# Performance work log

Hardware: AMD Instinct MI355X
Metric: run time of the kernel (lower is better)

The kernel has to match this reference:

```python
import jax, jax.numpy as jnp
import numpy as np

EPS = 1e-3
LOG2PI = float(np.log(2.0 * np.pi))

# dims
B, Z, Y, T, D = 32768, 256, 32, 64, 4  # batch, z_dim, y_dim, n_types, type_dim


def setup_inputs() -> dict:
    key = jax.random.key(0)
    ks = jax.random.split(key, 8)
    z = jax.random.normal(ks[0], (B, Z), dtype=jnp.float32)
    batch_x = jax.random.normal(ks[1], (B, T, D), dtype=jnp.float32)
    miss_list = jax.random.randint(ks[2], (B, T), 0, 2, dtype=jnp.int32)  # 1=observed, 0=missing
    data_mean = jax.random.normal(ks[3], (T, D), dtype=jnp.float32)
    data_var = jax.random.uniform(ks[4], (T, D), dtype=jnp.float32, minval=0.5, maxval=1.5)
    # weights init N(0, 0.005) as in the torch module; biases zero
    Wy = jax.random.normal(ks[5], (T * Y, Z), dtype=jnp.float32) * 0.005
    by = jnp.zeros((T * Y,), dtype=jnp.float32)
    Wm = jax.random.normal(ks[6], (T, D, Y), dtype=jnp.float32) * 0.005
    bm = jnp.zeros((T, D), dtype=jnp.float32)
    Wv = jax.random.normal(ks[7], (T, D, Y), dtype=jnp.float32) * 0.005
    bv = jnp.zeros((T, D), dtype=jnp.float32)
    return {"z": z, "batch_x": batch_x, "miss_list": miss_list,
            "data_mean": data_mean, "data_var": data_var,
            "Wy": Wy, "by": by, "Wm": Wm, "bm": bm, "Wv": Wv, "bv": bv}


def reference(z, batch_x, miss_list, data_mean, data_var, Wy, by, Wm, bm, Wv, bv):
    # y_layer: z -> [B, T*Y], grouped into per-type gamma slices [B, T, Y]
    y = z @ Wy.T + by
    gamma = y.reshape(y.shape[0], T, Y)

    mask = miss_list.astype(gamma.dtype)            # [B, T], 1=observed
    m3 = mask[:, :, None]                           # [B, T, 1]

    # per-type tiny linears (dynamic_partition + Linear + dynamic_stitch).
    # Numerically: same linear on all rows; missing rows are under no_grad,
    # realized here as stop_gradient on the missing partition.
    lin_m = jnp.einsum('bty,tdy->btd', gamma, Wm) + bm   # [B, T, D]
    lin_v = jnp.einsum('bty,tdy->btd', gamma, Wv) + bv
    est_mean = m3 * lin_m + (1.0 - m3) * jax.lax.stop_gradient(lin_m)
    est_var_raw = m3 * lin_v + (1.0 - m3) * jax.lax.stop_gradient(lin_v)

    # loglik_real: softplus variance, denormalize with data mean/var
    dvar = jnp.clip(data_var, EPS)
    est_var = jnp.clip(jax.nn.softplus(est_var_raw), EPS, 1e20)
    mean_x = jnp.sqrt(dvar) * est_mean + data_mean       # [B, T, D]
    var_x = dvar * est_var                               # [B, T, D]

    log_p = -0.5 * jnp.sum((batch_x - mean_x) ** 2 / var_x + jnp.log(var_x) + LOG2PI, axis=-1)  # [B, T]
    log_p_x = log_p * mask
    log_p_x_missing = log_p * (1.0 - mask)
    return (log_p_x, log_p_x_missing, mean_x, var_x)
```

## Files before the change

kernel.cpp:

```cpp
#include <hip/hip_runtime.h>


#define Bsz   32768
#define Tsz   64
#define Dsz   4
#define Ysz   32
#define Zsz   256
#define Nsz   512
#define BTtot (Bsz * Tsz)
#define EPS_  1e-3f
#define LOG2PI_ 1.8378770664093453f

#define BM       64
#define NT       512
#define ASTRIDE  264
#define LSTRIDE  528

typedef __attribute__((ext_vector_type(4))) float  f32x4;
typedef __attribute__((ext_vector_type(8))) short  short8;
typedef __attribute__((ext_vector_type(2))) unsigned int uint2v;

static __device__ __forceinline__ unsigned short f2bf(float f) {
    unsigned int u = __float_as_uint(f);
    return (unsigned short)((u + 0x7fffu + ((u >> 16) & 1u)) >> 16);
}
static __device__ __forceinline__ float bf2f(unsigned short h) {
    return __uint_as_float(((unsigned int)h) << 16);
}

__global__ __launch_bounds__(256)
void hidec_prep(const float* __restrict__ Wy, const float* __restrict__ by,
                const float* __restrict__ Wm, const float* __restrict__ bm,
                const float* __restrict__ Wv, const float* __restrict__ bv,
                unsigned short* __restrict__ weff, float* __restrict__ beff) {
    __shared__ float Ml[8][Ysz];
    __shared__ float byl[Ysz];
    const int t   = blockIdx.x;
    const int tid = threadIdx.x;
    {
        int j = tid >> 5, y = tid & 31;
        const float* src = (j < 4) ? Wm : Wv;
        Ml[j][y] = src[(t * Dsz + (j & 3)) * Ysz + y];
    }
    if (tid < Ysz) byl[tid] = by[t * Ysz + tid];
    __syncthreads();

    const int k = tid;
    const int kk = k >> 5, q = (k >> 3) & 3, je = k & 7;
    float wy[Ysz];
#pragma unroll
    for (int y = 0; y < Ysz; ++y)
        wy[y] = Wy[(size_t)(t * Ysz + y) * Zsz + k];
#pragma unroll
    for (int j = 0; j < 8; ++j) {
        float acc = 0.f;
#pragma unroll
        for (int y = 0; y < Ysz; ++y) acc = fmaf(Ml[j][y], wy[y], acc);
        int n   = t * 8 + j;
        int tau = n >> 4, c = n & 15;
        weff[((((tau * 8 + kk) * 4 + q) * 16 + c) * 8) + je] = f2bf(acc);
    }
    if (tid < 8) {
        int d = tid & 3;
        float s = ((tid < 4) ? bm : bv)[t * Dsz + d];
        for (int y = 0; y < Ysz; ++y) s = fmaf(byl[y], Ml[tid][y], s);
        beff[t * 8 + tid] = s;
    }
}

__global__ __launch_bounds__(NT, 4)
void hidec_main(const float* __restrict__ z, const float* __restrict__ bx,
                const int* __restrict__ miss, const float* __restrict__ dmean,
                const float* __restrict__ dvarp, const unsigned short* __restrict__ weff,
                const float* __restrict__ beff, float* __restrict__ out) {
    __shared__ unsigned short buf[BM * ASTRIDE];
    __shared__ float4 sqA[Tsz], dmA[Tsz], dcA[Tsz];
    __shared__ float  sldv[Tsz];
    __shared__ float  beffL[Nsz];

    const int tid  = threadIdx.x;
    const long row0 = (long)blockIdx.x * BM;

    if (tid < Tsz) {
        float4 dv4 = *(const float4*)(dvarp + tid * 4);
        float4 dm4 = *(const float4*)(dmean + tid * 4);
        float d0 = fmaxf(dv4.x, EPS_), d1 = fmaxf(dv4.y, EPS_);
        float d2 = fmaxf(dv4.z, EPS_), d3 = fmaxf(dv4.w, EPS_);
        sqA[tid] = (float4){sqrtf(d0), sqrtf(d1), sqrtf(d2), sqrtf(d3)};
        dmA[tid] = dm4;
        dcA[tid] = (float4){d0, d1, d2, d3};
        sldv[tid] = __logf(d0) + __logf(d1) + __logf(d2) + __logf(d3);
    }
    beffL[tid] = beff[tid];

    unsigned short* a_lds = buf;
#pragma unroll
    for (int i = 0; i < 8; ++i) {
        int idx4 = tid + i * NT;
        int r  = idx4 >> 6;
        int c4 = idx4 & 63;
        float4 v = *(const float4*)(z + (row0 + r) * Zsz + c4 * 4);
        uint2v p;
        p.x = (unsigned)f2bf(v.x) | ((unsigned)f2bf(v.y) << 16);
        p.y = (unsigned)f2bf(v.z) | ((unsigned)f2bf(v.w) << 16);
        *(uint2v*)&a_lds[r * ASTRIDE + c4 * 4] = p;
    }
    __syncthreads();

    const int lane = tid & 63;
    const int w    = tid >> 6;
    const int c    = lane & 15;
    const int q    = lane >> 4;

    f32x4 acc[16];
#pragma unroll
    for (int i = 0; i < 16; ++i) acc[i] = (f32x4){0.f, 0.f, 0.f, 0.f};

    const unsigned short* wp = weff + ((size_t)(w * 4) * 8) * 512 + lane * 8;

#pragma unroll
    for (int kk = 0; kk < 8; ++kk) {
        short8 b0 = *(const short8*)(wp + kk * 512 + 0 * 4096);
        short8 b1 = *(const short8*)(wp + kk * 512 + 1 * 4096);
        short8 b2 = *(const short8*)(wp + kk * 512 + 2 * 4096);
        short8 b3 = *(const short8*)(wp + kk * 512 + 3 * 4096);
        short8 a0 = *(const short8*)&a_lds[(0 * 16 + c) * ASTRIDE + kk * 32 + q * 8];
        short8 a1 = *(const short8*)&a_lds[(1 * 16 + c) * ASTRIDE + kk * 32 + q * 8];
        short8 a2 = *(const short8*)&a_lds[(2 * 16 + c) * ASTRIDE + kk * 32 + q * 8];
        short8 a3 = *(const short8*)&a_lds[(3 * 16 + c) * ASTRIDE + kk * 32 + q * 8];
        acc[0]  = __builtin_amdgcn_mfma_f32_16x16x32_bf16(a0, b0, acc[0],  0, 0, 0);
        acc[1]  = __builtin_amdgcn_mfma_f32_16x16x32_bf16(a1, b0, acc[1],  0, 0, 0);
        acc[2]  = __builtin_amdgcn_mfma_f32_16x16x32_bf16(a2, b0, acc[2],  0, 0, 0);
        acc[3]  = __builtin_amdgcn_mfma_f32_16x16x32_bf16(a3, b0, acc[3],  0, 0, 0);
        acc[4]  = __builtin_amdgcn_mfma_f32_16x16x32_bf16(a0, b1, acc[4],  0, 0, 0);
        acc[5]  = __builtin_amdgcn_mfma_f32_16x16x32_bf16(a1, b1, acc[5],  0, 0, 0);
        acc[6]  = __builtin_amdgcn_mfma_f32_16x16x32_bf16(a2, b1, acc[6],  0, 0, 0);
        acc[7]  = __builtin_amdgcn_mfma_f32_16x16x32_bf16(a3, b1, acc[7],  0, 0, 0);
        acc[8]  = __builtin_amdgcn_mfma_f32_16x16x32_bf16(a0, b2, acc[8],  0, 0, 0);
        acc[9]  = __builtin_amdgcn_mfma_f32_16x16x32_bf16(a1, b2, acc[9],  0, 0, 0);
        acc[10] = __builtin_amdgcn_mfma_f32_16x16x32_bf16(a2, b2, acc[10], 0, 0, 0);
        acc[11] = __builtin_amdgcn_mfma_f32_16x16x32_bf16(a3, b2, acc[11], 0, 0, 0);
        acc[12] = __builtin_amdgcn_mfma_f32_16x16x32_bf16(a0, b3, acc[12], 0, 0, 0);
        acc[13] = __builtin_amdgcn_mfma_f32_16x16x32_bf16(a1, b3, acc[13], 0, 0, 0);
        acc[14] = __builtin_amdgcn_mfma_f32_16x16x32_bf16(a2, b3, acc[14], 0, 0, 0);
        acc[15] = __builtin_amdgcn_mfma_f32_16x16x32_bf16(a3, b3, acc[15], 0, 0, 0);
    }
    __syncthreads();

    unsigned short* lin = buf;
#pragma unroll
    for (int ch = 0; ch < 2; ++ch) {
#pragma unroll
        for (int ti = 0; ti < 4; ++ti) {
            int n  = (w * 4 + ti) * 16 + c;
            float bb = beffL[n];
            int t  = n >> 3;
            int jj = n & 7;
#pragma unroll
            for (int rh = 0; rh < 2; ++rh) {
                int rt = ch * 2 + rh;
#pragma unroll
                for (int reg = 0; reg < 4; ++reg) {
                    int rl = rh * 16 + q * 4 + reg;
                    lin[rl * LSTRIDE + t * 8 + jj] = f2bf(acc[ti * 4 + rt][reg] + bb);
                }
            }
        }
        __syncthreads();

#pragma unroll
        for (int pp = 0; pp < 4; ++pp) {
            int task = pp * NT + tid;
            int t  = task & 63;
            int rl = task >> 6;
            long bt = (row0 + ch * 32 + rl) * Tsz + t;

            short8 l8 = *(const short8*)&lin[rl * LSTRIDE + t * 8];
            float lm[4], lv[4];
#pragma unroll
            for (int d = 0; d < 4; ++d) {
                lm[d] = bf2f((unsigned short)l8[d]);
                lv[d] = bf2f((unsigned short)l8[4 + d]);
            }

            float4 x4  = *(const float4*)(bx + bt * 4);
            float4 sq4 = sqA[t];
            float4 dm4 = dmA[t];
            float4 dc4 = dcA[t];
            float xa[4]  = {x4.x,  x4.y,  x4.z,  x4.w};
            float sqa[4] = {sq4.x, sq4.y, sq4.z, sq4.w};
            float dma[4] = {dm4.x, dm4.y, dm4.z, dm4.w};
            float dca[4] = {dc4.x, dc4.y, dc4.z, dc4.w};

            float mean_o[4], var_o[4];
            float s = sldv[t];
            float evp = 1.f;
#pragma unroll
            for (int d = 0; d < 4; ++d) {
                float mean = fmaf(sqa[d], lm[d], dma[d]);
                float v    = lv[d];
                float sp   = fmaxf(v, 0.f) + __logf(1.f + __expf(-fabsf(v)));
                float ev   = fminf(fmaxf(sp, EPS_), 1e20f);
                float var  = dca[d] * ev;
                float diff = xa[d] - mean;
                s = fmaf(diff * diff, __builtin_amdgcn_rcpf(var), s);
                evp *= ev;
                mean_o[d] = mean;
                var_o[d]  = var;
            }
            s += __logf(evp);
            float logp = -0.5f * (s + 4.f * LOG2PI_);
            float mk = (float)miss[bt];

            float lx = logp * mk;
            out[bt]         = lx;
            out[BTtot + bt] = logp - lx;

            *(float4*)(out + 2L * BTtot + bt * 4) =
                (float4){mean_o[0], mean_o[1], mean_o[2], mean_o[3]};
            *(float4*)(out + 6L * BTtot + bt * 4) =
                (float4){var_o[0], var_o[1], var_o[2], var_o[3]};
        }
        __syncthreads();
    }
}

extern "C" void kernel_launch(void* const* d_in, const int* in_sizes, int n_in,
                              void* d_out, int out_size, void* d_ws, size_t ws_size,
                              hipStream_t stream) {
    const float* z     = (const float*)d_in[0];
    const float* bx    = (const float*)d_in[1];
    const int*   miss  = (const int*)d_in[2];
    const float* dmean = (const float*)d_in[3];
    const float* dvar  = (const float*)d_in[4];
    const float* Wy    = (const float*)d_in[5];
    const float* by    = (const float*)d_in[6];
    const float* Wm    = (const float*)d_in[7];
    const float* bm    = (const float*)d_in[8];
    const float* Wv    = (const float*)d_in[9];
    const float* bv    = (const float*)d_in[10];
    float* out = (float*)d_out;

    unsigned short* weff = (unsigned short*)d_ws;
    float* beff = (float*)((char*)d_ws + (size_t)Nsz * Zsz * 2);

    hidec_prep<<<Tsz, Zsz, 0, stream>>>(Wy, by, Wm, bm, Wv, bv, weff, beff);
    hidec_main<<<Bsz / BM, NT, 0, stream>>>(z, bx, miss, dmean, dvar, weff, beff, out);
}
```

Baseline: 174.7 us.

## Use per-wave LDS epilogue staging to drop block barriers

Each wave now stages its own GEMM output columns (its 8 types across 32 rows) in a private LDS region and consumes them itself. This replaces the shared staging buffer and the block-wide __syncthreads calls with an lgkmcnt wait. It also uses the hardware packed bf16 conversion instruction instead of software rounding, and hoists the miss load earlier. The cost is extra LDS per block, which may reduce occupancy, and global store patterns per wave change (8 types by 8 rows instead of 64 contiguous types).

```diff
diff --git a/kernel.cpp b/kernel.cpp
--- a/kernel.cpp
+++ b/kernel.cpp
@@ -14,7 +14,7 @@
 #define BM       64
 #define NT       512
 #define ASTRIDE  264
-#define LSTRIDE  528
+#define LSTRIDE2 72
 
 typedef __attribute__((ext_vector_type(4))) float  f32x4;
 typedef __attribute__((ext_vector_type(8))) short  short8;
@@ -26,6 +26,11 @@
 }
 static __device__ __forceinline__ float bf2f(unsigned short h) {
     return __uint_as_float(((unsigned int)h) << 16);
+}
+static __device__ __forceinline__ unsigned int cvt_pk_bf16(float a, float b) {
+    unsigned int r;
+    asm("v_cvt_pk_bf16_f32 %0, %1, %2" : "=v"(r) : "v"(a), "v"(b));
+    return r;
 }
 
 __global__ __launch_bounds__(256)
@@ -73,7 +78,7 @@
                 const int* __restrict__ miss, const float* __restrict__ dmean,
                 const float* __restrict__ dvarp, const unsigned short* __restrict__ weff,
                 const float* __restrict__ beff, float* __restrict__ out) {
-    __shared__ unsigned short buf[BM * ASTRIDE];
+    __shared__ unsigned short buf[BM * ASTRIDE + 8 * 32 * LSTRIDE2];
     __shared__ float4 sqA[Tsz], dmA[Tsz], dcA[Tsz];
     __shared__ float  sldv[Tsz];
     __shared__ float  beffL[Nsz];
@@ -101,8 +106,8 @@
         int c4 = idx4 & 63;
         float4 v = *(const float4*)(z + (row0 + r) * Zsz + c4 * 4);
         uint2v p;
-        p.x = (unsigned)f2bf(v.x) | ((unsigned)f2bf(v.y) << 16);
-        p.y = (unsigned)f2bf(v.z) | ((unsigned)f2bf(v.w) << 16);
+        p.x = cvt_pk_bf16(v.x, v.y);
+        p.y = cvt_pk_bf16(v.z, v.w);
         *(uint2v*)&a_lds[r * ASTRIDE + c4 * 4] = p;
     }
     __syncthreads();
@@ -145,37 +150,40 @@
         acc[14] = __builtin_amdgcn_mfma_f32_16x16x32_bf16(a2, b3, acc[14], 0, 0, 0);
         acc[15] = __builtin_amdgcn_mfma_f32_16x16x32_bf16(a3, b3, acc[15], 0, 0, 0);
     }
-    __syncthreads();
-
-    unsigned short* lin = buf;
-#pragma unroll
-    for (int ch = 0; ch < 2; ++ch) {
+
+    unsigned short* lw = buf + BM * ASTRIDE + w * (32 * LSTRIDE2);
+
+    float bb[4];
+#pragma unroll
+    for (int ti = 0; ti < 4; ++ti) bb[ti] = beffL[w * 64 + ti * 16 + c];
+
+#pragma unroll
+    for (int h = 0; h < 2; ++h) {
 #pragma unroll
         for (int ti = 0; ti < 4; ++ti) {
-            int n  = (w * 4 + ti) * 16 + c;
-            float bb = beffL[n];
-            int t  = n >> 3;
-            int jj = n & 7;
+            int cb = ti * 16 + c;
 #pragma unroll
             for (int rh = 0; rh < 2; ++rh) {
-                int rt = ch * 2 + rh;
-#pragma unroll
-                for (int reg = 0; reg < 4; ++reg) {
-                    int rl = rh * 16 + q * 4 + reg;
-                    lin[rl * LSTRIDE + t * 8 + jj] = f2bf(acc[ti * 4 + rt][reg] + bb);
-                }
+                const f32x4 a = acc[ti * 4 + (2 * h + rh)];
+                unsigned int p01 = cvt_pk_bf16(a[0] + bb[ti], a[1] + bb[ti]);
+                unsigned int p23 = cvt_pk_bf16(a[2] + bb[ti], a[3] + bb[ti]);
+                int rbase = rh * 16 + q * 4;
+                lw[(rbase + 0) * LSTRIDE2 + cb] = (unsigned short)(p01 & 0xffffu);
+                lw[(rbase + 1) * LSTRIDE2 + cb] = (unsigned short)(p01 >> 16);
+                lw[(rbase + 2) * LSTRIDE2 + cb] = (unsigned short)(p23 & 0xffffu);
+                lw[(rbase + 3) * LSTRIDE2 + cb] = (unsigned short)(p23 >> 16);
             }
         }
-        __syncthreads();
-
-#pragma unroll
-        for (int pp = 0; pp < 4; ++pp) {
-            int task = pp * NT + tid;
-            int t  = task & 63;
-            int rl = task >> 6;
-            long bt = (row0 + ch * 32 + rl) * Tsz + t;
-
-            short8 l8 = *(const short8*)&lin[rl * LSTRIDE + t * 8];
+        asm volatile("s_waitcnt lgkmcnt(0)" ::: "memory");
+
+#pragma unroll
+        for (int p = 0; p < 4; ++p) {
+            int rloc = p * 8 + (lane >> 3);
+            int tl   = lane & 7;
+            int t    = w * 8 + tl;
+            long bt  = (row0 + h * 32 + rloc) * Tsz + t;
+
+            short8 l8 = *(const short8*)&lw[rloc * LSTRIDE2 + tl * 8];
             float lm[4], lv[4];
 #pragma unroll
             for (int d = 0; d < 4; ++d) {
@@ -184,6 +192,7 @@
             }
 
             float4 x4  = *(const float4*)(bx + bt * 4);
+            float mk   = (float)miss[bt];
             float4 sq4 = sqA[t];
             float4 dm4 = dmA[t];
             float4 dc4 = dcA[t];
@@ -210,7 +219,6 @@
             }
             s += __logf(evp);
             float logp = -0.5f * (s + 4.f * LOG2PI_);
-            float mk = (float)miss[bt];
 
             float lx = logp * mk;
             out[bt]         = lx;
@@ -221,7 +229,6 @@
             *(float4*)(out + 6L * BTtot + bt * 4) =
                 (float4){var_o[0], var_o[1], var_o[2], var_o[3]};
         }
-        __syncthreads();
     }
 }
 
```

After: 179.7 us. 2.9% more time.
